# Kernel tuning notes

Measured on AMD Instinct MI355X. Metric: run time of the kernel, lower is better.

Reference implementation:

```python
import jax, jax.numpy as jnp
import numpy as np

TEMPERATURE = 0.07


def setup_inputs() -> dict:
    key = jax.random.key(0)
    k1, k2 = jax.random.split(key)
    B, V, C, H, W = 4, 2, 128, 32, 32
    features = jax.random.normal(k1, (B, V, C, H, W), dtype=jnp.float32)
    # L2-normalize per-pixel feature vectors (channel dim), as contrastive
    # embeddings are in practice; the original exp() is unstabilized.
    features = features / jnp.linalg.norm(features, axis=2, keepdims=True)
    labels = jax.random.randint(k2, (B, V, H, W), 0, 4, dtype=jnp.int32)
    return {"features": features, "labels": labels}


def reference(features, labels):
    B, V, C, H, W = features.shape
    # torch.cat(torch.unbind(features, dim=1), dim=0): views stacked along batch
    cf = jnp.transpose(features, (1, 0, 2, 3, 4)).reshape(B * V, C, H, W)
    # kernels = cf.permute(0,2,3,1).reshape(-1, C, 1, 1); conv2d with 1x1 kernels
    # == pairwise dot products of per-pixel feature vectors.
    X = jnp.transpose(cf, (0, 2, 3, 1)).reshape(-1, C)  # [N, C], N = B*V*H*W
    N = X.shape[0]
    logits = (X @ X.T) / TEMPERATURE  # [N, N]

    lab = jnp.transpose(labels, (1, 0, 2, 3)).reshape(-1)  # [N]
    mask = (lab[:, None] == lab[None, :]).astype(logits.dtype)  # [N, N]
    logits_mask = 1.0 - jnp.eye(N, dtype=logits.dtype)  # zero the diagonal
    mask = mask * logits_mask

    exp_logits = jnp.exp(logits) * logits_mask
    log_prob = logits - jnp.log(jnp.sum(exp_logits, axis=1, keepdims=True))
    mean_log_prob_pos = jnp.sum(mask * log_prob, axis=1) / jnp.sum(mask, axis=1)
    loss = -mean_log_prob_pos  # [N]

    non_bg = (lab != 0).astype(logits.dtype)
    return jnp.sum(loss * non_bg) / jnp.sum(non_bg)
```

## Files before the change

### kernel.cpp

```cpp
#include <hip/hip_runtime.h>
#include <hip/hip_bf16.h>
#include <stdint.h>

typedef short bf16x8 __attribute__((ext_vector_type(8)));
typedef float f32x16 __attribute__((ext_vector_type(16)));

#define NROWS 8192
#define CDIM  128
#define TEMP  0.07f
#define C1F   20.6099291555566248f

__device__ __forceinline__ float bf2f(unsigned short u) {
  union { unsigned int i; float f; } x; x.i = ((unsigned int)u) << 16; return x.f;
}
__device__ __forceinline__ unsigned short f2bf(float f) {
  union { float f; unsigned int i; } x; x.f = f;
  unsigned int r = x.i + 0x7fffu + ((x.i >> 16) & 1u);
  return (unsigned short)(r >> 16);
}
__device__ __forceinline__ float fexp2(float x) {
#if __has_builtin(__builtin_amdgcn_exp2f)
  return __builtin_amdgcn_exp2f(x);
#else
  return exp2f(x);
#endif
}

__global__ __launch_bounds__(256) void k_pack(const float* __restrict__ F,
                                              unsigned short* __restrict__ Xb) {
  __shared__ float lds[128 * 33];
  const int g   = blockIdx.x >> 5;
  const int hw0 = (blockIdx.x & 31) << 5;
  const int tid = threadIdx.x;
#pragma unroll
  for (int p = 0; p < 16; ++p) {
    int c  = p * 8 + (tid >> 5);
    int hw = hw0 + (tid & 31);
    lds[c * 33 + (tid & 31)] = F[(g * 128 + c) * 1024 + hw];
  }
  __syncthreads();
#pragma unroll
  for (int p = 0; p < 16; ++p) {
    int hwl = p * 2 + (tid >> 7);
    int c   = tid & 127;
    int row = g * 1024 + hw0 + hwl;
    Xb[row * 128 + c] = f2bf(lds[c * 33 + hwl]);
  }
}

__global__ __launch_bounds__(256) void k_gsum(const unsigned short* __restrict__ Xb,
                                              const int* __restrict__ labels,
                                              float* __restrict__ G,
                                              int* __restrict__ hist) {
  const int tid    = threadIdx.x;
  const int lane   = tid & 63;
  const int rchunk = blockIdx.x >> 3;
  const int cbase  = (blockIdx.x & 7) * 16;
  const int cl     = tid & 15;
  const int rg     = tid >> 4;
  float a0 = 0.f, a1 = 0.f, a2 = 0.f, a3 = 0.f;
  const int nend = rchunk * 512 + 512;
  for (int n = rchunk * 512 + rg; n < nend; n += 16) {
    int   lab = labels[n];
    float v   = bf2f(Xb[n * 128 + cbase + cl]);
    a0 += (lab == 0) ? v : 0.f;
    a1 += (lab == 1) ? v : 0.f;
    a2 += (lab == 2) ? v : 0.f;
    a3 += (lab == 3) ? v : 0.f;
  }
  a0 += __shfl_xor(a0, 16, 64); a0 += __shfl_xor(a0, 32, 64);
  a1 += __shfl_xor(a1, 16, 64); a1 += __shfl_xor(a1, 32, 64);
  a2 += __shfl_xor(a2, 16, 64); a2 += __shfl_xor(a2, 32, 64);
  a3 += __shfl_xor(a3, 16, 64); a3 += __shfl_xor(a3, 32, 64);
  if (lane < 16) {
    int c = cbase + lane;
    atomicAdd(&G[0 * 128 + c], a0);
    atomicAdd(&G[1 * 128 + c], a1);
    atomicAdd(&G[2 * 128 + c], a2);
    atomicAdd(&G[3 * 128 + c], a3);
  }
  if (blockIdx.x == 0) {
    int h0 = 0, h1 = 0, h2 = 0, h3 = 0;
    for (int n = tid; n < NROWS; n += 256) {
      int lab = labels[n];
      h0 += (lab == 0); h1 += (lab == 1); h2 += (lab == 2); h3 += (lab == 3);
    }
    for (int m = 1; m < 64; m <<= 1) {
      h0 += __shfl_xor(h0, m, 64); h1 += __shfl_xor(h1, m, 64);
      h2 += __shfl_xor(h2, m, 64); h3 += __shfl_xor(h3, m, 64);
    }
    if (lane == 0) {
      atomicAdd(&hist[0], h0); atomicAdd(&hist[1], h1);
      atomicAdd(&hist[2], h2); atomicAdd(&hist[3], h3);
    }
  }
}

__global__ __launch_bounds__(256, 4) void k_main(const unsigned short* __restrict__ Xb,
                                                 float* __restrict__ S) {
  __shared__ int4 ldsB[2][16 * 33];
  const int tid      = threadIdx.x;
  const int lane     = tid & 63;
  const int wave     = tid >> 6;
  const int rowBlock = blockIdx.x >> 4;
  const int split    = blockIdx.x & 15;
  const int r0       = rowBlock * 128 + wave * 32;
  const int col0     = split * 512;
  const int m        = lane & 31;
  const int half     = lane >> 5;

  bf16x8 afrag[8];
#pragma unroll
  for (int s = 0; s < 8; ++s)
    afrag[s] = *(const bf16x8*)(Xb + (r0 + m) * CDIM + (half + 2 * s) * 8);

  float accS[16];
#pragma unroll
  for (int r = 0; r < 16; ++r) accS[r] = 0.f;

  const int n_l = tid >> 3;
  const int bq  = tid & 7;
  const unsigned short* src = Xb + (col0 + n_l) * CDIM + bq * 16;
  int4 v0 = *(const int4*)src;
  int4 v1 = *(const int4*)(src + 8);
  ldsB[0][(2 * bq) * 33 + n_l]     = v0;
  ldsB[0][(2 * bq + 1) * 33 + n_l] = v1;
  src += 32 * CDIM;
  v0 = *(const int4*)src;
  v1 = *(const int4*)(src + 8);

  for (int t = 0; t < 16; ++t) {
    __syncthreads();
    if (t < 15) {
      ldsB[(t + 1) & 1][(2 * bq) * 33 + n_l]     = v0;
      ldsB[(t + 1) & 1][(2 * bq + 1) * 33 + n_l] = v1;
    }
    if (t < 14) {
      src += 32 * CDIM;
      v0 = *(const int4*)src;
      v1 = *(const int4*)(src + 8);
    }
    const int cur = t & 1;
    f32x16 acc;
#pragma unroll
    for (int r = 0; r < 16; ++r) acc[r] = 0.f;
#pragma unroll
    for (int s = 0; s < 8; ++s) {
      bf16x8 bfrag = *(const bf16x8*)&ldsB[cur][(half + 2 * s) * 33 + m];
      acc = __builtin_amdgcn_mfma_f32_32x32x16_bf16(afrag[s], bfrag, acc, 0, 0, 0);
    }
    const int colbase = col0 + t * 32;
    if (r0 == colbase) {
      const int colg = colbase + m;
#pragma unroll
      for (int r = 0; r < 16; ++r) {
        int   row = r0 + (r & 3) + 8 * (r >> 2) + 4 * half;
        float arg = (row == colg) ? -1e30f : acc[r] * C1F;
        accS[r] += fexp2(arg);
      }
    } else {
#pragma unroll
      for (int r = 0; r < 16; ++r) accS[r] += fexp2(acc[r] * C1F);
    }
  }

#pragma unroll
  for (int r = 0; r < 16; ++r) {
    float v = accS[r];
    v += __shfl_xor(v, 1, 64);
    v += __shfl_xor(v, 2, 64);
    v += __shfl_xor(v, 4, 64);
    v += __shfl_xor(v, 8, 64);
    v += __shfl_xor(v, 16, 64);
    accS[r] = v;
  }
  if (m == 0) {
#pragma unroll
    for (int r = 0; r < 16; ++r) {
      int row = r0 + (r & 3) + 8 * (r >> 2) + 4 * half;
      atomicAdd(&S[row], accS[r]);
    }
  }
}

__global__ __launch_bounds__(256) void k_loss(const unsigned short* __restrict__ Xb,
                                              const int* __restrict__ labels,
                                              const float* __restrict__ S,
                                              const float* __restrict__ G,
                                              const int* __restrict__ hist,
                                              float* __restrict__ sumLoss) {
  const int i   = blockIdx.x * 256 + threadIdx.x;
  const int lab = labels[i];
  const float* g = G + lab * 128;
  const unsigned short* x = Xb + i * CDIM;
  float dot = 0.f, nrm = 0.f;
#pragma unroll
  for (int cc = 0; cc < 16; ++cc) {
    int4 q = *(const int4*)(x + cc * 8);
    const unsigned int* qs = (const unsigned int*)&q;
#pragma unroll
    for (int j = 0; j < 4; ++j) {
      unsigned int u = qs[j];
      float lo = __uint_as_float(u << 16);
      float hi = __uint_as_float(u & 0xffff0000u);
      int   ci = cc * 8 + j * 2;
      dot += lo * g[ci] + hi * g[ci + 1];
      nrm += lo * lo + hi * hi;
    }
  }
  float Si   = S[i];
  float cnt  = (float)(hist[lab] - 1);
  float loss = logf(Si) - (dot - nrm) / (TEMP * cnt);
  float contrib = (lab != 0) ? loss : 0.f;
  for (int mm = 1; mm < 64; mm <<= 1) contrib += __shfl_xor(contrib, mm, 64);
  __shared__ float ws4[4];
  if ((threadIdx.x & 63) == 0) ws4[threadIdx.x >> 6] = contrib;
  __syncthreads();
  if (threadIdx.x == 0) atomicAdd(sumLoss, ws4[0] + ws4[1] + ws4[2] + ws4[3]);
}

__global__ void k_final(const float* __restrict__ sumLoss,
                        const int* __restrict__ hist,
                        float* __restrict__ out) {
  out[0] = sumLoss[0] / (float)(NROWS - hist[0]);
}

extern "C" void kernel_launch(void* const* d_in, const int* in_sizes, int n_in,
                              void* d_out, int out_size, void* d_ws, size_t ws_size,
                              hipStream_t stream) {
  const float* F      = (const float*)d_in[0];
  const int*   labels = (const int*)d_in[1];
  char* ws = (char*)d_ws;

  unsigned short* Xb      = (unsigned short*)ws;
  const size_t    offS    = (size_t)NROWS * CDIM * 2;
  float*          S       = (float*)(ws + offS);
  float*          G       = (float*)(ws + offS + 32768);
  int*            hist    = (int*)(ws + offS + 32768 + 2048);
  float*          sumLoss = (float*)(ws + offS + 32768 + 2048 + 16);

  hipMemsetAsync(ws + offS, 0, 32768 + 2048 + 16 + 4, stream);

  hipLaunchKernelGGL(k_pack, dim3(256), dim3(256), 0, stream, F, Xb);
  hipLaunchKernelGGL(k_gsum, dim3(128), dim3(256), 0, stream, Xb, labels, G, hist);
  hipLaunchKernelGGL(k_main, dim3(1024), dim3(256), 0, stream, Xb, S);
  hipLaunchKernelGGL(k_loss, dim3(32), dim3(256), 0, stream, Xb, labels, S, G, hist, sumLoss);
  hipLaunchKernelGGL(k_final, dim3(1), dim3(1), 0, stream, sumLoss, hist, (float*)d_out);
}
```

Baseline: 110.2 us.

## Fuse launches: zero in pack, merge gsum into main, final via ticket

```diff
diff --git a/kernel.cpp b/kernel.cpp
--- a/kernel.cpp
+++ b/kernel.cpp
@@ -9,6 +9,14 @@
 #define CDIM  128
 #define TEMP  0.07f
 #define C1F   20.6099291555566248f
+
+#define OFF_S    0
+#define OFF_G    32768
+#define OFF_HIST (32768 + 2048)
+#define OFF_SUM  (32768 + 2048 + 16)
+#define OFF_TKT  (32768 + 2048 + 16 + 4)
+#define ZBYTES   (32768 + 2048 + 16 + 4 + 4)
+#define ZWORDS   (ZBYTES / 4)
 
 __device__ __forceinline__ float bf2f(unsigned short u) {
   union { unsigned int i; float f; } x; x.i = ((unsigned int)u) << 16; return x.f;
@@ -27,11 +35,16 @@
 }
 
 __global__ __launch_bounds__(256) void k_pack(const float* __restrict__ F,
-                                              unsigned short* __restrict__ Xb) {
+                                              unsigned short* __restrict__ Xb,
+                                              float* __restrict__ zbase) {
+  const int tid = threadIdx.x;
+  {
+    int idx = blockIdx.x * 256 + tid;
+    if (idx < ZWORDS) zbase[idx] = 0.0f;
+  }
   __shared__ float lds[128 * 33];
   const int g   = blockIdx.x >> 5;
   const int hw0 = (blockIdx.x & 31) << 5;
-  const int tid = threadIdx.x;
 #pragma unroll
   for (int p = 0; p < 16; ++p) {
     int c  = p * 8 + (tid >> 5);
@@ -48,62 +61,64 @@
   }
 }
 
-__global__ __launch_bounds__(256) void k_gsum(const unsigned short* __restrict__ Xb,
-                                              const int* __restrict__ labels,
-                                              float* __restrict__ G,
-                                              int* __restrict__ hist) {
-  const int tid    = threadIdx.x;
-  const int lane   = tid & 63;
-  const int rchunk = blockIdx.x >> 3;
-  const int cbase  = (blockIdx.x & 7) * 16;
-  const int cl     = tid & 15;
-  const int rg     = tid >> 4;
-  float a0 = 0.f, a1 = 0.f, a2 = 0.f, a3 = 0.f;
-  const int nend = rchunk * 512 + 512;
-  for (int n = rchunk * 512 + rg; n < nend; n += 16) {
-    int   lab = labels[n];
-    float v   = bf2f(Xb[n * 128 + cbase + cl]);
-    a0 += (lab == 0) ? v : 0.f;
-    a1 += (lab == 1) ? v : 0.f;
-    a2 += (lab == 2) ? v : 0.f;
-    a3 += (lab == 3) ? v : 0.f;
-  }
-  a0 += __shfl_xor(a0, 16, 64); a0 += __shfl_xor(a0, 32, 64);
-  a1 += __shfl_xor(a1, 16, 64); a1 += __shfl_xor(a1, 32, 64);
-  a2 += __shfl_xor(a2, 16, 64); a2 += __shfl_xor(a2, 32, 64);
-  a3 += __shfl_xor(a3, 16, 64); a3 += __shfl_xor(a3, 32, 64);
-  if (lane < 16) {
-    int c = cbase + lane;
-    atomicAdd(&G[0 * 128 + c], a0);
-    atomicAdd(&G[1 * 128 + c], a1);
-    atomicAdd(&G[2 * 128 + c], a2);
-    atomicAdd(&G[3 * 128 + c], a3);
-  }
-  if (blockIdx.x == 0) {
-    int h0 = 0, h1 = 0, h2 = 0, h3 = 0;
-    for (int n = tid; n < NROWS; n += 256) {
-      int lab = labels[n];
-      h0 += (lab == 0); h1 += (lab == 1); h2 += (lab == 2); h3 += (lab == 3);
-    }
-    for (int m = 1; m < 64; m <<= 1) {
-      h0 += __shfl_xor(h0, m, 64); h1 += __shfl_xor(h1, m, 64);
-      h2 += __shfl_xor(h2, m, 64); h3 += __shfl_xor(h3, m, 64);
-    }
-    if (lane == 0) {
-      atomicAdd(&hist[0], h0); atomicAdd(&hist[1], h1);
-      atomicAdd(&hist[2], h2); atomicAdd(&hist[3], h3);
-    }
-  }
-}
-
 __global__ __launch_bounds__(256, 4) void k_main(const unsigned short* __restrict__ Xb,
-                                                 float* __restrict__ S) {
-  __shared__ int4 ldsB[2][16 * 33];
-  const int tid      = threadIdx.x;
-  const int lane     = tid & 63;
+                                                 const int* __restrict__ labels,
+                                                 float* __restrict__ S,
+                                                 float* __restrict__ G,
+                                                 int* __restrict__ hist) {
+  __shared__ int4 ldsB[2][2][16 * 33];
+  const int bid = blockIdx.x;
+  const int tid = threadIdx.x;
+  const int lane = tid & 63;
+
+  if (bid < 128) {
+    const int rchunk = bid >> 3;
+    const int cbase  = (bid & 7) * 16;
+    const int cl     = tid & 15;
+    const int rg     = tid >> 4;
+    float a0 = 0.f, a1 = 0.f, a2 = 0.f, a3 = 0.f;
+    const int nend = rchunk * 512 + 512;
+    for (int n = rchunk * 512 + rg; n < nend; n += 16) {
+      int   lab = labels[n];
+      float v   = bf2f(Xb[n * 128 + cbase + cl]);
+      a0 += (lab == 0) ? v : 0.f;
+      a1 += (lab == 1) ? v : 0.f;
+      a2 += (lab == 2) ? v : 0.f;
+      a3 += (lab == 3) ? v : 0.f;
+    }
+    a0 += __shfl_xor(a0, 16, 64); a0 += __shfl_xor(a0, 32, 64);
+    a1 += __shfl_xor(a1, 16, 64); a1 += __shfl_xor(a1, 32, 64);
+    a2 += __shfl_xor(a2, 16, 64); a2 += __shfl_xor(a2, 32, 64);
+    a3 += __shfl_xor(a3, 16, 64); a3 += __shfl_xor(a3, 32, 64);
+    if (lane < 16) {
+      int c = cbase + lane;
+      atomicAdd(&G[0 * 128 + c], a0);
+      atomicAdd(&G[1 * 128 + c], a1);
+      atomicAdd(&G[2 * 128 + c], a2);
+      atomicAdd(&G[3 * 128 + c], a3);
+    }
+    if (bid == 0) {
+      int h0 = 0, h1 = 0, h2 = 0, h3 = 0;
+      for (int n = tid; n < NROWS; n += 256) {
+        int lab = labels[n];
+        h0 += (lab == 0); h1 += (lab == 1); h2 += (lab == 2); h3 += (lab == 3);
+      }
+      for (int mm = 1; mm < 64; mm <<= 1) {
+        h0 += __shfl_xor(h0, mm, 64); h1 += __shfl_xor(h1, mm, 64);
+        h2 += __shfl_xor(h2, mm, 64); h3 += __shfl_xor(h3, mm, 64);
+      }
+      if (lane == 0) {
+        atomicAdd(&hist[0], h0); atomicAdd(&hist[1], h1);
+        atomicAdd(&hist[2], h2); atomicAdd(&hist[3], h3);
+      }
+    }
+    return;
+  }
+
+  const int b        = bid - 128;
   const int wave     = tid >> 6;
-  const int rowBlock = blockIdx.x >> 4;
-  const int split    = blockIdx.x & 15;
+  const int rowBlock = b >> 4;
+  const int split    = b & 15;
   const int r0       = rowBlock * 128 + wave * 32;
   const int col0     = split * 512;
   const int m        = lane & 31;
@@ -123,44 +138,58 @@
   const unsigned short* src = Xb + (col0 + n_l) * CDIM + bq * 16;
   int4 v0 = *(const int4*)src;
   int4 v1 = *(const int4*)(src + 8);
-  ldsB[0][(2 * bq) * 33 + n_l]     = v0;
-  ldsB[0][(2 * bq + 1) * 33 + n_l] = v1;
-  src += 32 * CDIM;
+  int4 v2 = *(const int4*)(src + 32 * CDIM);
+  int4 v3 = *(const int4*)(src + 32 * CDIM + 8);
+  ldsB[0][0][(2 * bq) * 33 + n_l]     = v0;
+  ldsB[0][0][(2 * bq + 1) * 33 + n_l] = v1;
+  ldsB[0][1][(2 * bq) * 33 + n_l]     = v2;
+  ldsB[0][1][(2 * bq + 1) * 33 + n_l] = v3;
+  src += 64 * CDIM;
   v0 = *(const int4*)src;
   v1 = *(const int4*)(src + 8);
-
-  for (int t = 0; t < 16; ++t) {
+  v2 = *(const int4*)(src + 32 * CDIM);
+  v3 = *(const int4*)(src + 32 * CDIM + 8);
+
+  for (int t = 0; t < 8; ++t) {
     __syncthreads();
-    if (t < 15) {
-      ldsB[(t + 1) & 1][(2 * bq) * 33 + n_l]     = v0;
-      ldsB[(t + 1) & 1][(2 * bq + 1) * 33 + n_l] = v1;
-    }
-    if (t < 14) {
-      src += 32 * CDIM;
+    if (t < 7) {
+      const int nb = (t + 1) & 1;
+      ldsB[nb][0][(2 * bq) * 33 + n_l]     = v0;
+      ldsB[nb][0][(2 * bq + 1) * 33 + n_l] = v1;
+      ldsB[nb][1][(2 * bq) * 33 + n_l]     = v2;
+      ldsB[nb][1][(2 * bq + 1) * 33 + n_l] = v3;
+    }
+    if (t < 6) {
+      src += 64 * CDIM;
       v0 = *(const int4*)src;
       v1 = *(const int4*)(src + 8);
+      v2 = *(const int4*)(src + 32 * CDIM);
+      v3 = *(const int4*)(src + 32 * CDIM + 8);
     }
     const int cur = t & 1;
-    f32x16 acc;
-#pragma unroll
-    for (int r = 0; r < 16; ++r) acc[r] = 0.f;
-#pragma unroll
-    for (int s = 0; s < 8; ++s) {
-      bf16x8 bfrag = *(const bf16x8*)&ldsB[cur][(half + 2 * s) * 33 + m];
-      acc = __builtin_amdgcn_mfma_f32_32x32x16_bf16(afrag[s], bfrag, acc, 0, 0, 0);
-    }
-    const int colbase = col0 + t * 32;
-    if (r0 == colbase) {
-      const int colg = colbase + m;
-#pragma unroll
-      for (int r = 0; r < 16; ++r) {
-        int   row = r0 + (r & 3) + 8 * (r >> 2) + 4 * half;
-        float arg = (row == colg) ? -1e30f : acc[r] * C1F;
-        accS[r] += fexp2(arg);
-      }
-    } else {
-#pragma unroll
-      for (int r = 0; r < 16; ++r) accS[r] += fexp2(acc[r] * C1F);
+#pragma unroll
+    for (int u = 0; u < 2; ++u) {
+      f32x16 acc;
+#pragma unroll
+      for (int r = 0; r < 16; ++r) acc[r] = 0.f;
+#pragma unroll
+      for (int s = 0; s < 8; ++s) {
+        bf16x8 bfrag = *(const bf16x8*)&ldsB[cur][u][(half + 2 * s) * 33 + m];
+        acc = __builtin_amdgcn_mfma_f32_32x32x16_bf16(afrag[s], bfrag, acc, 0, 0, 0);
+      }
+      const int colbase = col0 + t * 64 + u * 32;
+      if (r0 == colbase) {
+        const int colg = colbase + m;
+#pragma unroll
+        for (int r = 0; r < 16; ++r) {
+          int   row = r0 + (r & 3) + 8 * (r >> 2) + 4 * half;
+          float arg = (row == colg) ? -1e30f : acc[r] * C1F;
+          accS[r] += fexp2(arg);
+        }
+      } else {
+#pragma unroll
+        for (int r = 0; r < 16; ++r) accS[r] += fexp2(acc[r] * C1F);
+      }
     }
   }
 
@@ -188,7 +217,9 @@
                                               const float* __restrict__ S,
                                               const float* __restrict__ G,
                                               const int* __restrict__ hist,
-                                              float* __restrict__ sumLoss) {
+                                              float* __restrict__ sumLoss,
+                                              int* __restrict__ ticket,
+                                              float* __restrict__ out) {
   const int i   = blockIdx.x * 256 + threadIdx.x;
   const int lab = labels[i];
   const float* g = G + lab * 128;
@@ -216,13 +247,15 @@
   __shared__ float ws4[4];
   if ((threadIdx.x & 63) == 0) ws4[threadIdx.x >> 6] = contrib;
   __syncthreads();
-  if (threadIdx.x == 0) atomicAdd(sumLoss, ws4[0] + ws4[1] + ws4[2] + ws4[3]);
-}
-
-__global__ void k_final(const float* __restrict__ sumLoss,
-                        const int* __restrict__ hist,
-                        float* __restrict__ out) {
-  out[0] = sumLoss[0] / (float)(NROWS - hist[0]);
+  if (threadIdx.x == 0) {
+    atomicAdd(sumLoss, ws4[0] + ws4[1] + ws4[2] + ws4[3]);
+    __threadfence();
+    int t = atomicAdd(ticket, 1);
+    if (t == 31) {
+      float total = atomicAdd(sumLoss, 0.0f);
+      out[0] = total / (float)(NROWS - hist[0]);
+    }
+  }
 }
 
 extern "C" void kernel_launch(void* const* d_in, const int* in_sizes, int n_in,
@@ -234,16 +267,14 @@
 
   unsigned short* Xb      = (unsigned short*)ws;
   const size_t    offS    = (size_t)NROWS * CDIM * 2;
-  float*          S       = (float*)(ws + offS);
-  float*          G       = (float*)(ws + offS + 32768);
-  int*            hist    = (int*)(ws + offS + 32768 + 2048);
-  float*          sumLoss = (float*)(ws + offS + 32768 + 2048 + 16);
-
-  hipMemsetAsync(ws + offS, 0, 32768 + 2048 + 16 + 4, stream);
-
-  hipLaunchKernelGGL(k_pack, dim3(256), dim3(256), 0, stream, F, Xb);
-  hipLaunchKernelGGL(k_gsum, dim3(128), dim3(256), 0, stream, Xb, labels, G, hist);
-  hipLaunchKernelGGL(k_main, dim3(1024), dim3(256), 0, stream, Xb, S);
-  hipLaunchKernelGGL(k_loss, dim3(32), dim3(256), 0, stream, Xb, labels, S, G, hist, sumLoss);
-  hipLaunchKernelGGL(k_final, dim3(1), dim3(1), 0, stream, sumLoss, hist, (float*)d_out);
-}
+  float*          S       = (float*)(ws + offS + OFF_S);
+  float*          G       = (float*)(ws + offS + OFF_G);
+  int*            hist    = (int*)(ws + offS + OFF_HIST);
+  float*          sumLoss = (float*)(ws + offS + OFF_SUM);
+  int*            ticket  = (int*)(ws + offS + OFF_TKT);
+
+  hipLaunchKernelGGL(k_pack, dim3(256), dim3(256), 0, stream, F, Xb, S);
+  hipLaunchKernelGGL(k_main, dim3(1152), dim3(256), 0, stream, Xb, labels, S, G, hist);
+  hipLaunchKernelGGL(k_loss, dim3(32), dim3(256), 0, stream, Xb, labels, S, G, hist,
+                     sumLoss, ticket, (float*)d_out);
+}
```

Measured after the change: 99.76 us. -9.4%, faster.
